# Optimization experiments

Measured on AMD Instinct MI355X. Metric: run time of the kernel, lower is better.

## Reference

```python
import jax, jax.numpy as jnp
import numpy as np

NUM_HEADS = 16
KERNEL_SIZE = 13


def setup_inputs() -> dict:
    key = jax.random.key(0)
    ks = jax.random.split(key, 6)
    B, L, C = 4, 4096, 512
    H, K = NUM_HEADS, KERNEL_SIZE
    x = jax.random.normal(ks[0], (B, L, C), dtype=jnp.float32)
    qkv_w = jax.random.normal(ks[1], (C, 3 * C), dtype=jnp.float32) * 0.02
    qkv_b = jnp.zeros((3 * C,), dtype=jnp.float32)
    rpb = jax.random.normal(ks[2], (H, 2 * K - 1), dtype=jnp.float32) * 0.02
    proj_w = jax.random.normal(ks[3], (C, C), dtype=jnp.float32) * 0.02
    proj_b = jnp.zeros((C,), dtype=jnp.float32)
    return {"x": x, "qkv_w": qkv_w, "qkv_b": qkv_b, "rpb": rpb,
            "proj_w": proj_w, "proj_b": proj_b}


def reference(x, qkv_w, qkv_b, rpb, proj_w, proj_b):
    B, L, C = x.shape
    H, K = NUM_HEADS, KERNEL_SIZE
    hd = C // H
    scale = hd ** -0.5
    kh = K // 2

    # qkv projection -> q,k,v each [B,H,L,hd]
    qkv = (x @ qkv_w + qkv_b).reshape(B, L, 3, H, hd).transpose(2, 0, 3, 1, 4)
    q, k, v = qkv[0] * scale, qkv[1], qkv[2]

    # NATTEN window: start index clamped so window stays in-bounds
    pos = jnp.arange(L)
    ni = jnp.clip(pos - kh, 0, L - K)              # [L] window start per query
    idx = ni[:, None] + jnp.arange(K)[None, :]     # [L,K] key positions
    # rpb index: (key_pos - query_pos) + (K-1)
    rpb_idx = (ni - pos + (K - 1))[:, None] + jnp.arange(K)[None, :]  # [L,K]

    k_win = k[:, :, idx, :]                        # [B,H,L,K,hd]
    v_win = v[:, :, idx, :]                        # [B,H,L,K,hd]

    attn = jnp.einsum('bhld,bhlkd->bhlk', q, k_win) + rpb[:, rpb_idx][None]
    attn = jax.nn.softmax(attn, axis=-1)

    out = jnp.einsum('bhlk,bhlkd->bhld', attn, v_win)  # [B,H,L,hd]
    out = out.transpose(0, 2, 1, 3).reshape(B, L, C)
    return out @ proj_w + proj_b
```

## Files before the change

kernel.cpp:

```cpp
#include <hip/hip_runtime.h>
#include <hip/hip_bf16.h>
#include <stdint.h>


typedef __attribute__((ext_vector_type(8))) short short8;
typedef __attribute__((ext_vector_type(4))) float f32x4;
typedef __attribute__((ext_vector_type(8))) unsigned short u16x8;
typedef __attribute__((ext_vector_type(4))) float float4v;

#define NB 4
#define NL 4096
#define NC 512
#define NH 16
#define HD 32
#define KW 13
#define KHALF 6
#define NM (NB*NL)

__device__ __forceinline__ float b2f(unsigned short u) {
  union { unsigned int i; float f; } x; x.i = ((unsigned int)u) << 16; return x.f;
}
__device__ __forceinline__ unsigned short f2b(float f) {
  __hip_bfloat16 h = __float2bfloat16(f);
  return __builtin_bit_cast(unsigned short, h);
}
__device__ __forceinline__ void gll16(const unsigned short* g, unsigned short* l) {
  __builtin_amdgcn_global_load_lds(
      (const __attribute__((address_space(1))) void*)g,
      (__attribute__((address_space(3))) void*)l, 16, 0, 0);
}

__global__ __launch_bounds__(256) void cvt_f32_bf16(const float* __restrict__ in,
                                                    unsigned short* __restrict__ out) {
  long i = (long)blockIdx.x * 256 + threadIdx.x;
  const float4v* in4 = (const float4v*)in;
  float4v a = in4[i * 2];
  float4v b = in4[i * 2 + 1];
  u16x8 u;
  u[0] = f2b(a.x); u[1] = f2b(a.y); u[2] = f2b(a.z); u[3] = f2b(a.w);
  u[4] = f2b(b.x); u[5] = f2b(b.y); u[6] = f2b(b.z); u[7] = f2b(b.w);
  ((u16x8*)out)[i] = u;
}

__global__ __launch_bounds__(256) void transpose_bf16(const float* __restrict__ in,
                                                      unsigned short* __restrict__ out,
                                                      int R, int C) {
  __shared__ float t[32][33];
  int c0 = blockIdx.x * 32;
  int r0 = blockIdx.y * 32;
  int tx = threadIdx.x;
  int ty = threadIdx.y;
  #pragma unroll
  for (int i = ty; i < 32; i += 8)
    t[i][tx] = in[(long)(r0 + i) * C + c0 + tx];
  __syncthreads();
  #pragma unroll
  for (int i = ty; i < 32; i += 8)
    out[(long)(c0 + i) * R + r0 + tx] = f2b(t[tx][i]);
}

template<int OUT_BF16>
__global__ __launch_bounds__(256)
void gemm_bt(const unsigned short* __restrict__ A,
             const unsigned short* __restrict__ BT,
             const float* __restrict__ bias,
             void* __restrict__ Cout,
             int M, int N, int K, int tilesN) {
  __shared__ __align__(16) unsigned short sA[128 * 32];
  __shared__ __align__(16) unsigned short sB[128 * 32];

  int tid  = threadIdx.x;
  int bid  = blockIdx.x;
  int tm   = bid / tilesN, tn = bid % tilesN;
  long mBase = (long)tm * 128;
  long nBase = (long)tn * 128;
  int lane = tid & 63, wave = tid >> 6;
  int wm = wave >> 1, wn = wave & 1;
  int lr = lane & 15, lk = lane >> 4;

  f32x4 acc[4][4];
  #pragma unroll
  for (int i = 0; i < 4; ++i)
    #pragma unroll
    for (int j = 0; j < 4; ++j) acc[i][j] = (f32x4){0.f, 0.f, 0.f, 0.f};

  int rA = tid >> 2;
  int cA = (tid & 3) * 8;
  const unsigned short* gA0 = A  + (mBase + rA)      * (long)K + cA;
  const unsigned short* gA1 = A  + (mBase + 64 + rA) * (long)K + cA;
  const unsigned short* gB0 = BT + (nBase + rA)      * (long)K + cA;
  const unsigned short* gB1 = BT + (nBase + 64 + rA) * (long)K + cA;
  unsigned short* lA0 = sA + tid * 8;
  unsigned short* lA1 = sA + 2048 + tid * 8;
  unsigned short* lB0 = sB + tid * 8;
  unsigned short* lB1 = sB + 2048 + tid * 8;

  const short8* sA8 = (const short8*)sA;
  const short8* sB8 = (const short8*)sB;

  for (int kt = 0; kt < K; kt += 32) {
    gll16(gA0 + kt, lA0);
    gll16(gA1 + kt, lA1);
    gll16(gB0 + kt, lB0);
    gll16(gB1 + kt, lB1);
    __syncthreads();

    short8 af[4], bf[4];
    #pragma unroll
    for (int i = 0; i < 4; ++i) af[i] = sA8[(wm * 64 + i * 16 + lr) * 4 + lk];
    #pragma unroll
    for (int j = 0; j < 4; ++j) bf[j] = sB8[(wn * 64 + j * 16 + lr) * 4 + lk];
    #pragma unroll
    for (int i = 0; i < 4; ++i)
      #pragma unroll
      for (int j = 0; j < 4; ++j)
        acc[i][j] = __builtin_amdgcn_mfma_f32_16x16x32_bf16(af[i], bf[j], acc[i][j], 0, 0, 0);
    __syncthreads();
  }

  long rowb = mBase + wm * 64 + (lane >> 4) * 4;
  int  colb = (int)nBase + wn * 64 + lr;
  if (OUT_BF16) {
    unsigned short* C = (unsigned short*)Cout;
    #pragma unroll
    for (int i = 0; i < 4; ++i)
      #pragma unroll
      for (int j = 0; j < 4; ++j) {
        int col = colb + j * 16;
        float bv = bias[col];
        #pragma unroll
        for (int r = 0; r < 4; ++r)
          C[(rowb + i * 16 + r) * (long)N + col] = f2b(acc[i][j][r] + bv);
      }
  } else {
    float* C = (float*)Cout;
    #pragma unroll
    for (int i = 0; i < 4; ++i)
      #pragma unroll
      for (int j = 0; j < 4; ++j) {
        int col = colb + j * 16;
        float bv = bias[col];
        #pragma unroll
        for (int r = 0; r < 4; ++r)
          C[(rowb + i * 16 + r) * (long)N + col] = acc[i][j][r] + bv;
      }
  }
}

__global__ __launch_bounds__(256)
void natt(const unsigned short* __restrict__ qkv, const float* __restrict__ rpb,
          unsigned short* __restrict__ out) {
  int tid = blockIdx.x * 256 + threadIdx.x;
  int h = tid & 15;
  int l = (tid >> 4) & (NL - 1);
  int b = tid >> 16;
  const float scale = 0.17677669529663687f;

  long qb = ((long)(b * NL + l) * 3) * NC + h * HD;
  float q[HD];
  {
    const u16x8* q8 = (const u16x8*)(qkv + qb);
    #pragma unroll
    for (int w = 0; w < 4; ++w) {
      u16x8 u = q8[w];
      #pragma unroll
      for (int e = 0; e < 8; ++e) q[w * 8 + e] = b2f(u[e]) * scale;
    }
  }

  int ni = l - KHALF;
  if (ni < 0) ni = 0;
  if (ni > NL - KW) ni = NL - KW;
  const float* rb = rpb + h * (2 * KW - 1) + (ni - l + KW - 1);

  float p[KW];
  float mx = -1e30f;
  #pragma unroll
  for (int j = 0; j < KW; ++j) {
    long kb = ((long)(b * NL + ni + j) * 3 + 1) * NC + h * HD;
    const u16x8* k8 = (const u16x8*)(qkv + kb);
    float s = 0.f;
    #pragma unroll
    for (int w = 0; w < 4; ++w) {
      u16x8 u = k8[w];
      #pragma unroll
      for (int e = 0; e < 8; ++e) s += q[w * 8 + e] * b2f(u[e]);
    }
    s += rb[j];
    p[j] = s;
    mx = fmaxf(mx, s);
  }

  float sum = 0.f;
  #pragma unroll
  for (int j = 0; j < KW; ++j) { p[j] = __expf(p[j] - mx); sum += p[j]; }
  float inv = 1.0f / sum;

  float o[HD];
  #pragma unroll
  for (int d = 0; d < HD; ++d) o[d] = 0.f;
  #pragma unroll
  for (int j = 0; j < KW; ++j) {
    long vb = ((long)(b * NL + ni + j) * 3 + 2) * NC + h * HD;
    const u16x8* v8 = (const u16x8*)(qkv + vb);
    float wj = p[j] * inv;
    #pragma unroll
    for (int w = 0; w < 4; ++w) {
      u16x8 u = v8[w];
      #pragma unroll
      for (int e = 0; e < 8; ++e) o[w * 8 + e] += wj * b2f(u[e]);
    }
  }

  unsigned short* op = out + (long)(b * NL + l) * NC + h * HD;
  #pragma unroll
  for (int w = 0; w < 4; ++w) {
    u16x8 u;
    #pragma unroll
    for (int e = 0; e < 8; ++e) u[e] = f2b(o[w * 8 + e]);
    *((u16x8*)(op + w * 8)) = u;
  }
}

extern "C" void kernel_launch(void* const* d_in, const int* in_sizes, int n_in,
                              void* d_out, int out_size, void* d_ws, size_t ws_size,
                              hipStream_t stream) {
  const float* x      = (const float*)d_in[0];
  const float* qkv_w  = (const float*)d_in[1];
  const float* qkv_b  = (const float*)d_in[2];
  const float* rpb    = (const float*)d_in[3];
  const float* proj_w = (const float*)d_in[4];
  const float* proj_b = (const float*)d_in[5];
  float* out = (float*)d_out;

  char* ws = (char*)d_ws;
  unsigned short* xb     = (unsigned short*)(ws);
  unsigned short* qkvwT  = (unsigned short*)(ws + 16777216);
  unsigned short* projwT = (unsigned short*)(ws + 18350080);
  unsigned short* qkvo   = (unsigned short*)(ws + 18874368);
  unsigned short* attno  = (unsigned short*)(ws + 69206016);

  cvt_f32_bf16<<<dim3(4096), dim3(256), 0, stream>>>(x, xb);
  transpose_bf16<<<dim3(48, 16), dim3(32, 8), 0, stream>>>(qkv_w, qkvwT, 512, 1536);
  transpose_bf16<<<dim3(16, 16), dim3(32, 8), 0, stream>>>(proj_w, projwT, 512, 512);
  gemm_bt<1><<<dim3(128 * 12), dim3(256), 0, stream>>>(xb, qkvwT, qkv_b, qkvo,
                                                       NM, 1536, 512, 12);
  natt<<<dim3(1024), dim3(256), 0, stream>>>(qkvo, rpb, attno);
  gemm_bt<0><<<dim3(128 * 4), dim3(256), 0, stream>>>(attno, projwT, proj_b, out,
                                                      NM, 512, 512, 4);
}
```

Baseline: 114.8 us.

## Replace 128x128 GEMM with double-buffered 256x256 tile pipelined GEMM

Replaces the simple 128x128 tiled GEMM, which loads and syncs every 32-wide k step, with a 512-thread 256x256 tile kernel. It uses 64-wide k tiles, double-buffered LDS via global_load_lds, an XOR-swizzled LDS layout, interleaved load/MFMA phases with explicit vmcnt waits and setprio, and an XCD-aware block remap. The aim is more data reuse per tile and load latency hidden behind MFMA work. The output GEMM now launches only 128 blocks, which may underfill the GPU, and the loop hardcodes 8 k-tiles, so it assumes K=512.

Result: faster. 109.2 us (-4.9%).

```diff
diff --git a/kernel.cpp b/kernel.cpp
--- a/kernel.cpp
+++ b/kernel.cpp
@@ -59,90 +59,171 @@
     out[(long)(c0 + i) * R + r0 + tx] = f2b(t[tx][i]);
 }
 
+
+__device__ __forceinline__ void stage_half(const unsigned short* __restrict__ G,
+                                           long rowBase, int K, int kt,
+                                           unsigned short* ldsDst, int tid) {
+  int r  = tid >> 3;
+  int ch = (tid & 7) ^ (r & 7);
+  const unsigned short* s0 = G + (rowBase + r) * (long)K + kt * 64 + ch * 8;
+  gll16(s0, ldsDst + tid * 8);
+  gll16(s0 + 64 * (long)K, ldsDst + 4096 + tid * 8);
+}
+
+#define BAR() __builtin_amdgcn_s_barrier()
+#define LGK0() asm volatile("s_waitcnt lgkmcnt(0)" ::: "memory")
+#define VM(N) asm volatile("s_waitcnt vmcnt(" #N ")" ::: "memory")
+
+#define DS_A(BUF, QM) do { \
+  const char* _ba = (const char*)(lds + (BUF)*16384 + wm*8192); \
+  _Pragma("unroll") for (int ii = 0; ii < 4; ++ii) { \
+    int _row = ((QM)*4+ii)*16 + lr; \
+    _Pragma("unroll") for (int kb = 0; kb < 2; ++kb) \
+      af[ii][kb] = *(const short8*)(_ba + _row*128 + (((kb*4+lk) ^ lr7) * 16)); \
+  } \
+} while (0)
+
+#define DS_B(BUF, QN, BF) do { \
+  const char* _bb = (const char*)(lds + 32768 + (BUF)*16384 + (wn>>1)*8192); \
+  _Pragma("unroll") for (int jj = 0; jj < 2; ++jj) { \
+    int _row = (wn&1)*64 + ((QN)*2+jj)*16 + lr; \
+    _Pragma("unroll") for (int kb = 0; kb < 2; ++kb) \
+      BF[jj][kb] = *(const short8*)(_bb + _row*128 + (((kb*4+lk) ^ lr7) * 16)); \
+  } \
+} while (0)
+
+#define MMA(QM, QN, BF) do { \
+  __builtin_amdgcn_s_setprio(1); \
+  _Pragma("unroll") for (int ii = 0; ii < 4; ++ii) \
+    _Pragma("unroll") for (int jj = 0; jj < 2; ++jj) \
+      _Pragma("unroll") for (int kb = 0; kb < 2; ++kb) \
+        acc[(QM)*4+ii][(QN)*2+jj] = __builtin_amdgcn_mfma_f32_16x16x32_bf16( \
+            af[ii][kb], BF[jj][kb], acc[(QM)*4+ii][(QN)*2+jj], 0, 0, 0); \
+  __builtin_amdgcn_s_setprio(0); \
+} while (0)
+
 template<int OUT_BF16>
-__global__ __launch_bounds__(256)
-void gemm_bt(const unsigned short* __restrict__ A,
+__global__ __launch_bounds__(512, 2)
+void gemm256(const unsigned short* __restrict__ A,
              const unsigned short* __restrict__ BT,
              const float* __restrict__ bias,
              void* __restrict__ Cout,
              int M, int N, int K, int tilesN) {
-  __shared__ __align__(16) unsigned short sA[128 * 32];
-  __shared__ __align__(16) unsigned short sB[128 * 32];
-
-  int tid  = threadIdx.x;
-  int bid  = blockIdx.x;
-  int tm   = bid / tilesN, tn = bid % tilesN;
-  long mBase = (long)tm * 128;
-  long nBase = (long)tn * 128;
+  __shared__ __align__(16) unsigned short lds[65536];
+
+  int tid = threadIdx.x;
+  int nwg = gridDim.x;
+  int cpx = nwg >> 3;
+  int wg  = ((int)blockIdx.x & 7) * cpx + ((int)blockIdx.x >> 3);
+  int tm = wg / tilesN, tn = wg % tilesN;
+  long mBase = (long)tm * 256;
+  long nBase = (long)tn * 256;
+
   int lane = tid & 63, wave = tid >> 6;
-  int wm = wave >> 1, wn = wave & 1;
-  int lr = lane & 15, lk = lane >> 4;
-
-  f32x4 acc[4][4];
-  #pragma unroll
-  for (int i = 0; i < 4; ++i)
+  int wm = wave >> 2;
+  int wn = wave & 3;
+  int lr = lane & 15, lk = lane >> 4, lr7 = lr & 7;
+
+  unsigned short* A0h0 = lds;
+  unsigned short* A0h1 = lds + 8192;
+  unsigned short* A1h0 = lds + 16384;
+  unsigned short* A1h1 = lds + 16384 + 8192;
+  unsigned short* B0h0 = lds + 32768;
+  unsigned short* B0h1 = lds + 32768 + 8192;
+  unsigned short* B1h0 = lds + 32768 + 16384;
+  unsigned short* B1h1 = lds + 32768 + 16384 + 8192;
+
+  f32x4 acc[8][4];
+  #pragma unroll
+  for (int i = 0; i < 8; ++i)
     #pragma unroll
     for (int j = 0; j < 4; ++j) acc[i][j] = (f32x4){0.f, 0.f, 0.f, 0.f};
 
-  int rA = tid >> 2;
-  int cA = (tid & 3) * 8;
-  const unsigned short* gA0 = A  + (mBase + rA)      * (long)K + cA;
-  const unsigned short* gA1 = A  + (mBase + 64 + rA) * (long)K + cA;
-  const unsigned short* gB0 = BT + (nBase + rA)      * (long)K + cA;
-  const unsigned short* gB1 = BT + (nBase + 64 + rA) * (long)K + cA;
-  unsigned short* lA0 = sA + tid * 8;
-  unsigned short* lA1 = sA + 2048 + tid * 8;
-  unsigned short* lB0 = sB + tid * 8;
-  unsigned short* lB1 = sB + 2048 + tid * 8;
-
-  const short8* sA8 = (const short8*)sA;
-  const short8* sB8 = (const short8*)sB;
-
-  for (int kt = 0; kt < K; kt += 32) {
-    gll16(gA0 + kt, lA0);
-    gll16(gA1 + kt, lA1);
-    gll16(gB0 + kt, lB0);
-    gll16(gB1 + kt, lB1);
-    __syncthreads();
-
-    short8 af[4], bf[4];
-    #pragma unroll
-    for (int i = 0; i < 4; ++i) af[i] = sA8[(wm * 64 + i * 16 + lr) * 4 + lk];
-    #pragma unroll
-    for (int j = 0; j < 4; ++j) bf[j] = sB8[(wn * 64 + j * 16 + lr) * 4 + lk];
-    #pragma unroll
-    for (int i = 0; i < 4; ++i)
-      #pragma unroll
-      for (int j = 0; j < 4; ++j)
-        acc[i][j] = __builtin_amdgcn_mfma_f32_16x16x32_bf16(af[i], bf[j], acc[i][j], 0, 0, 0);
-    __syncthreads();
-  }
-
-  long rowb = mBase + wm * 64 + (lane >> 4) * 4;
+  short8 af[4][2], bf0[2][2], bf1[2][2];
+
+  stage_half(BT, nBase,       K, 0, B0h0, tid);
+  stage_half(BT, nBase + 128, K, 0, B0h1, tid);
+  stage_half(A,  mBase,       K, 0, A0h0, tid);
+  stage_half(A,  mBase + 128, K, 0, A0h1, tid);
+  stage_half(BT, nBase,       K, 1, B1h0, tid);
+  stage_half(BT, nBase + 128, K, 1, B1h1, tid);
+  VM(4);
+  BAR();
+
+  #pragma unroll 1
+  for (int it = 0; it < 4; ++it) {
+    int kt = it * 2;
+    bool s2 = (kt + 2) < 8;
+    bool s3 = (kt + 3) < 8;
+
+    DS_A(0, 0);
+    DS_B(0, 0, bf0);
+    stage_half(A, mBase, K, kt + 1, A1h0, tid);
+    BAR(); LGK0();
+    MMA(0, 0, bf0);
+    BAR();
+    DS_B(0, 1, bf1);
+    stage_half(A, mBase + 128, K, kt + 1, A1h1, tid);
+    BAR(); LGK0();
+    MMA(0, 1, bf1);
+    BAR();
+    DS_A(0, 1);
+    if (s2) stage_half(BT, nBase, K, kt + 2, B0h0, tid);
+    BAR(); LGK0();
+    MMA(1, 1, bf1);
+    BAR();
+    if (s2) { stage_half(BT, nBase + 128, K, kt + 2, B0h1, tid); VM(4); }
+    else    { VM(0); }
+    BAR();
+    MMA(1, 0, bf0);
+    BAR();
+    DS_A(1, 0);
+    DS_B(1, 0, bf0);
+    if (s2) stage_half(A, mBase, K, kt + 2, A0h0, tid);
+    BAR(); LGK0();
+    MMA(0, 0, bf0);
+    BAR();
+    DS_B(1, 1, bf1);
+    if (s2) stage_half(A, mBase + 128, K, kt + 2, A0h1, tid);
+    BAR(); LGK0();
+    MMA(0, 1, bf1);
+    BAR();
+    DS_A(1, 1);
+    if (s3) stage_half(BT, nBase, K, kt + 3, B1h0, tid);
+    BAR(); LGK0();
+    MMA(1, 1, bf1);
+    BAR();
+    if (s3) { stage_half(BT, nBase + 128, K, kt + 3, B1h1, tid); VM(4); }
+    BAR();
+    MMA(1, 0, bf0);
+    BAR();
+  }
+
+  long rowb = mBase + wm * 128 + (lane >> 4) * 4;
   int  colb = (int)nBase + wn * 64 + lr;
   if (OUT_BF16) {
     unsigned short* C = (unsigned short*)Cout;
     #pragma unroll
-    for (int i = 0; i < 4; ++i)
-      #pragma unroll
-      for (int j = 0; j < 4; ++j) {
-        int col = colb + j * 16;
+    for (int mi = 0; mi < 8; ++mi)
+      #pragma unroll
+      for (int nj = 0; nj < 4; ++nj) {
+        int col = colb + nj * 16;
         float bv = bias[col];
         #pragma unroll
         for (int r = 0; r < 4; ++r)
-          C[(rowb + i * 16 + r) * (long)N + col] = f2b(acc[i][j][r] + bv);
+          C[(rowb + mi * 16 + r) * (long)N + col] = f2b(acc[mi][nj][r] + bv);
       }
   } else {
     float* C = (float*)Cout;
     #pragma unroll
-    for (int i = 0; i < 4; ++i)
-      #pragma unroll
-      for (int j = 0; j < 4; ++j) {
-        int col = colb + j * 16;
+    for (int mi = 0; mi < 8; ++mi)
+      #pragma unroll
+      for (int nj = 0; nj < 4; ++nj) {
+        int col = colb + nj * 16;
         float bv = bias[col];
         #pragma unroll
         for (int r = 0; r < 4; ++r)
-          C[(rowb + i * 16 + r) * (long)N + col] = acc[i][j][r] + bv;
+          C[(rowb + mi * 16 + r) * (long)N + col] = acc[mi][nj][r] + bv;
       }
   }
 }
@@ -243,9 +324,9 @@
   cvt_f32_bf16<<<dim3(4096), dim3(256), 0, stream>>>(x, xb);
   transpose_bf16<<<dim3(48, 16), dim3(32, 8), 0, stream>>>(qkv_w, qkvwT, 512, 1536);
   transpose_bf16<<<dim3(16, 16), dim3(32, 8), 0, stream>>>(proj_w, projwT, 512, 512);
-  gemm_bt<1><<<dim3(128 * 12), dim3(256), 0, stream>>>(xb, qkvwT, qkv_b, qkvo,
-                                                       NM, 1536, 512, 12);
+  gemm256<1><<<dim3(384), dim3(512), 0, stream>>>(xb, qkvwT, qkv_b, qkvo,
+                                                  NM, 1536, 512, 6);
   natt<<<dim3(1024), dim3(256), 0, stream>>>(qkvo, rpb, attno);
-  gemm_bt<0><<<dim3(128 * 4), dim3(256), 0, stream>>>(attno, projwT, proj_b, out,
-                                                      NM, 512, 512, 4);
-}
+  gemm256<0><<<dim3(128), dim3(512), 0, stream>>>(attno, projwT, proj_b, out,
+                                                  NM, 512, 512, 2);
+}
```
